# Kernel tuning notes

Hardware: AMD Instinct MI355X
Metric: run time of the kernel (lower is better)

The kernel has to match this reference:

```python
import jax, jax.numpy as jnp
import numpy as np

PIXEL_THRESHOLD = 0.4
FRACTION_THRESHOLD = 0.03
NUM_CLASSES = 20  # cls_idx in [0, 20)
N, H, W = 100, 640, 1280


def setup_inputs() -> dict:
    key = jax.random.key(0)
    k1, k2, k3 = jax.random.split(key, 3)
    cls_prob = jax.random.uniform(k1, (N,), dtype=jnp.float32)
    mask_prob = jax.random.normal(k2, (N, H, W), dtype=jnp.float32)
    cls_idx = jax.random.randint(k3, (N,), 0, NUM_CLASSES, dtype=jnp.int32)
    return {"cls_prob": cls_prob, "mask_prob": mask_prob, "cls_idx": cls_idx}


def reference(cls_prob, mask_prob, cls_idx):
    """Greedy confidence-sorted panoptic mask merging (mask_removal).

    Returns:
      keep:       [N] bool  - whether each (sorted) instance was kept
      kept_masks: [N,H,W]   - assigned raw mask probs (zeros where suppressed/unassigned)
      order:      [N] int   - descending-confidence permutation applied
    """
    # Sort by class confidence, descending (matches np.argsort(...)[::-1])
    order = jnp.argsort(cls_prob)[::-1]
    mp_raw = mask_prob[order]                      # [N,H,W] pre-softmax copy
    mp_soft = jax.nn.softmax(mp_raw, axis=0)       # softmax across instances per pixel
    ci = cls_idx[order]                            # [N]

    h, w = mp_raw.shape[-2:]
    pan0 = jnp.zeros((h, w), dtype=mp_raw.dtype)            # panoptic_image
    mimg0 = jnp.zeros((NUM_CLASSES + 1, h, w), dtype=mp_raw.dtype)  # per-class mask_image

    def step(carry, inp):
        pan, mimg = carry
        prob_s, prob_raw, cidx = inp
        logit = (prob_s >= PIXEL_THRESHOLD).astype(prob_s.dtype)  # binarized mask
        mask_sum = logit.sum()
        curr = mimg[cidx]                                         # [H,W]
        overlap_cnt = ((curr >= 1) & (logit == 1)).sum().astype(prob_s.dtype)
        overlap = overlap_cnt / jnp.maximum(mask_sum, 1.0)
        trivial = logit.max() == logit.min()  # all-zero or all-one mask
        keep = (~trivial) & (mask_sum > 0) & (overlap <= FRACTION_THRESHOLD)
        assign = (pan == 0) & (logit == 1) & keep                 # unclaimed pixels
        kept_mask = jnp.where(assign, prob_raw, 0.0)
        pan = jnp.where(assign, 1.0, pan)
        mimg = mimg.at[cidx].add(jnp.where(assign, logit, 0.0))
        return (pan, mimg), (keep, kept_mask)

    (_, _), (keep, kept_masks) = jax.lax.scan(step, (pan0, mimg0), (mp_soft, mp_raw, ci))
    return keep, kept_masks, order
```

## Files before the change

### kernel.cpp

```cpp
#include <hip/hip_runtime.h>

#define N_INST 100
#define HW_PIX 819200
#define NPAIR (N_INST * N_INST)

struct alignas(16) Ent { int p; int ab; float ra; float rb; };

__global__ __launch_bounds__(128) void k0_sort(
    const float* __restrict__ cls_prob,
    const int* __restrict__ cls_idx,
    int* __restrict__ order,
    int* __restrict__ cls_sorted,
    float* __restrict__ out_order) {
  __shared__ float v[N_INST];
  __shared__ int ordl[N_INST];
  int t = threadIdx.x;
  if (t < N_INST) v[t] = cls_prob[t];
  __syncthreads();
  if (t < N_INST) {
    float mv = v[t];
    int r = 0;
    for (int j = 0; j < N_INST; ++j) {
      float vj = v[j];
      r += (vj > mv) || (vj == mv && j > t);
    }
    ordl[r] = t;
  }
  __syncthreads();
  if (t < N_INST) {
    int o = ordl[t];
    order[t] = o;
    cls_sorted[t] = cls_idx[o];
    out_order[t] = (float)o;
  }
}

__global__ __launch_bounds__(256) void k1_cand(
    const float* __restrict__ mp,
    const int* __restrict__ order,
    unsigned int* __restrict__ masksum,
    unsigned int* __restrict__ paircnt,
    unsigned int* __restrict__ nc,
    Ent* __restrict__ list) {
  int p = blockIdx.x * 256 + threadIdx.x;
  float x[N_INST];
#pragma unroll
  for (int k = 0; k < N_INST; ++k)
    x[k] = mp[(size_t)order[k] * HW_PIX + p];
  float m = x[0];
#pragma unroll
  for (int k = 1; k < N_INST; ++k) m = fmaxf(m, x[k]);
  float denom = 0.0f, e1 = -1.0f, e2 = -1.0f, r1 = 0.0f, r2 = 0.0f;
  int s1 = 0, s2 = 0;
#pragma unroll
  for (int k = 0; k < N_INST; ++k) {
    float e = expf(x[k] - m);
    denom += e;
    if (e > e1)      { e2 = e1; s2 = s1; r2 = r1; e1 = e; s1 = k; r1 = x[k]; }
    else if (e > e2) { e2 = e;  s2 = k;  r2 = x[k]; }
  }
  bool c1 = (e1 / denom) >= 0.4f;
  bool c2 = (e2 / denom) >= 0.4f;
  if (c1) {
    int a = s1, b = 255;
    float ra = r1, rb = 0.0f;
    atomicAdd(&masksum[s1], 1u);
    if (c2) {
      atomicAdd(&masksum[s2], 1u);
      if (s2 < s1) { a = s2; ra = r2; b = s1; rb = r1; }
      else         { b = s2; rb = r2; }
      atomicAdd(&paircnt[a * N_INST + b], 1u);
    }
    unsigned idx = atomicAdd(nc, 1u);
    Ent e; e.p = p; e.ab = a | (b << 8); e.ra = ra; e.rb = rb;
    list[idx] = e;
  }
}

__global__ __launch_bounds__(256) void k2_keep(
    const unsigned int* __restrict__ paircnt,
    const unsigned int* __restrict__ masksum,
    const int* __restrict__ cls_sorted,
    unsigned long long* __restrict__ keepmask,
    float* __restrict__ out_keep) {
  __shared__ unsigned int pl[NPAIR];
  __shared__ unsigned int ms[N_INST];
  __shared__ int cl[N_INST];
  for (int i = threadIdx.x; i < NPAIR; i += 256) pl[i] = paircnt[i];
  if (threadIdx.x < N_INST) {
    ms[threadIdx.x] = masksum[threadIdx.x];
    cl[threadIdx.x] = cls_sorted[threadIdx.x];
  }
  __syncthreads();
  if (threadIdx.x < 64) {
    int l = threadIdx.x;
    int j2 = l + 64;
    int cA = cl[l];
    int cB = (j2 < N_INST) ? cl[j2] : -1;
    bool kA = false, kB = false;
    unsigned long long km0 = 0, km1 = 0;
    for (int s = 0; s < N_INST; ++s) {
      int cs = cl[s];
      unsigned int ov = 0;
      if (l < s && kA && cA == cs) ov += pl[l * N_INST + s];
      if (j2 < s && kB && cB == cs) ov += pl[j2 * N_INST + s];
#pragma unroll
      for (int off = 32; off >= 1; off >>= 1) ov += __shfl_xor((int)ov, off);
      unsigned int m_s = ms[s];
      float overlap = (float)ov / fmaxf((float)m_s, 1.0f);
      bool keep = (m_s > 0u) && (m_s < (unsigned)HW_PIX) && (overlap <= 0.03f);
      if (keep) { if (s < 64) km0 |= 1ull << s; else km1 |= 1ull << (s - 64); }
      if (s == l)  kA = keep;
      if (s == j2) kB = keep;
    }
    if (l == 0) { keepmask[0] = km0; keepmask[1] = km1; }
    out_keep[l] = kA ? 1.0f : 0.0f;
    if (j2 < N_INST) out_keep[j2] = kB ? 1.0f : 0.0f;
  }
}

__global__ __launch_bounds__(256) void k3_scatter(
    const unsigned int* __restrict__ nc,
    const Ent* __restrict__ list,
    const unsigned long long* __restrict__ keepmask,
    float* __restrict__ out_masks) {
  unsigned long long km0 = keepmask[0], km1 = keepmask[1];
  unsigned n = *nc;
  for (unsigned i = blockIdx.x * 256 + threadIdx.x; i < n; i += gridDim.x * 256) {
    Ent e = list[i];
    int a = e.ab & 0xFF;
    int b = (e.ab >> 8) & 0xFF;
    bool ka = (a < 64) ? (((km0 >> a) & 1ull) != 0)
                       : ((a < N_INST) && (((km1 >> (a - 64)) & 1ull) != 0));
    bool kb = (b < 64) ? (((km0 >> b) & 1ull) != 0)
                       : ((b < N_INST) && (((km1 >> (b - 64)) & 1ull) != 0));
    if (ka)      out_masks[(size_t)a * HW_PIX + e.p] = e.ra;
    else if (kb) out_masks[(size_t)b * HW_PIX + e.p] = e.rb;
  }
}

extern "C" void kernel_launch(void* const* d_in, const int* in_sizes, int n_in,
                              void* d_out, int out_size, void* d_ws, size_t ws_size,
                              hipStream_t stream) {
  const float* cls_prob = (const float*)d_in[0];
  const float* mp       = (const float*)d_in[1];
  const int*   cls_idx  = (const int*)d_in[2];
  float* out = (float*)d_out;

  char* ws = (char*)d_ws;
  int* order                   = (int*)(ws + 0);
  int* cls_sorted              = (int*)(ws + 400);
  unsigned long long* keepmask = (unsigned long long*)(ws + 800);
  unsigned int* nc             = (unsigned int*)(ws + 1024);
  unsigned int* masksum        = (unsigned int*)(ws + 2048);
  unsigned int* paircnt        = (unsigned int*)(ws + 4096);
  Ent* list                    = (Ent*)(ws + 65536);

  float* out_keep  = out;
  float* out_masks = out + N_INST;
  float* out_order = out + N_INST + (size_t)N_INST * HW_PIX;

  hipMemsetAsync(ws + 1024, 0, 4096 - 1024 + 40000, stream);
  hipMemsetAsync(out_masks, 0, (size_t)N_INST * HW_PIX * sizeof(float), stream);

  k0_sort<<<1, 128, 0, stream>>>(cls_prob, cls_idx, order, cls_sorted, out_order);
  k1_cand<<<HW_PIX / 256, 256, 0, stream>>>(mp, order, masksum, paircnt, nc, list);
  k2_keep<<<1, 256, 0, stream>>>(paircnt, masksum, cls_sorted, keepmask, out_keep);
  k3_scatter<<<128, 256, 0, stream>>>(nc, list, keepmask, out_masks);
}
```

Before: 610.7 us.

## Replace memset+scatter with dense per-pixel records and a full vectorized output write

The compacted candidate list built with a global atomic counter is replaced by dense per-pixel records holding the winning pair and its raw values. The final kernel now writes the whole output mask tensor with float4 stores, filling zeros itself, so the separate 328MB memset disappears. The candidate kernel also caches the order in shared memory and finds the top-2 on raw logits, so only one exp pass is needed. The cost is extra per-pixel record traffic (about 10MB) in exchange for dropping one full pass over the output.

Result: slower. 889.7 us (+45.7%).

```diff
diff --git a/kernel.cpp b/kernel.cpp
--- a/kernel.cpp
+++ b/kernel.cpp
@@ -3,8 +3,6 @@
 #define N_INST 100
 #define HW_PIX 819200
 #define NPAIR (N_INST * N_INST)
-
-struct alignas(16) Ent { int p; int ab; float ra; float rb; };
 
 __global__ __launch_bounds__(128) void k0_sort(
     const float* __restrict__ cls_prob,
@@ -40,41 +38,46 @@
     const int* __restrict__ order,
     unsigned int* __restrict__ masksum,
     unsigned int* __restrict__ paircnt,
-    unsigned int* __restrict__ nc,
-    Ent* __restrict__ list) {
+    unsigned int* __restrict__ ab_rec,
+    float2* __restrict__ rv_rec) {
+  __shared__ int so[N_INST];
+  if (threadIdx.x < N_INST) so[threadIdx.x] = order[threadIdx.x];
+  __syncthreads();
+
   int p = blockIdx.x * 256 + threadIdx.x;
+
   float x[N_INST];
-#pragma unroll
-  for (int k = 0; k < N_INST; ++k)
-    x[k] = mp[(size_t)order[k] * HW_PIX + p];
-  float m = x[0];
-#pragma unroll
-  for (int k = 1; k < N_INST; ++k) m = fmaxf(m, x[k]);
-  float denom = 0.0f, e1 = -1.0f, e2 = -1.0f, r1 = 0.0f, r2 = 0.0f;
+  float m1 = -3.0e38f, m2 = -3.0e38f;
   int s1 = 0, s2 = 0;
 #pragma unroll
   for (int k = 0; k < N_INST; ++k) {
-    float e = expf(x[k] - m);
-    denom += e;
-    if (e > e1)      { e2 = e1; s2 = s1; r2 = r1; e1 = e; s1 = k; r1 = x[k]; }
-    else if (e > e2) { e2 = e;  s2 = k;  r2 = x[k]; }
+    float xv = mp[(size_t)so[k] * HW_PIX + p];
+    x[k] = xv;
+    if (xv > m1)      { m2 = m1; s2 = s1; m1 = xv; s1 = k; }
+    else if (xv > m2) { m2 = xv; s2 = k; }
   }
-  bool c1 = (e1 / denom) >= 0.4f;
-  bool c2 = (e2 / denom) >= 0.4f;
+  float denom = 0.0f;
+#pragma unroll
+  for (int k = 0; k < N_INST; ++k) denom += expf(x[k] - m1);
+
+  bool c1 = (1.0f / denom) >= 0.4f;
+  bool c2 = (expf(m2 - m1) / denom) >= 0.4f;
+
+  unsigned int abv = 0xFFFFu;
   if (c1) {
     int a = s1, b = 255;
-    float ra = r1, rb = 0.0f;
+    float ra = m1, rb = 0.0f;
     atomicAdd(&masksum[s1], 1u);
     if (c2) {
       atomicAdd(&masksum[s2], 1u);
-      if (s2 < s1) { a = s2; ra = r2; b = s1; rb = r1; }
-      else         { b = s2; rb = r2; }
+      if (s2 < s1) { a = s2; ra = m2; b = s1; rb = m1; }
+      else         { b = s2; rb = m2; }
       atomicAdd(&paircnt[a * N_INST + b], 1u);
     }
-    unsigned idx = atomicAdd(nc, 1u);
-    Ent e; e.p = p; e.ab = a | (b << 8); e.ra = ra; e.rb = rb;
-    list[idx] = e;
+    abv = (unsigned)a | ((unsigned)b << 8);
+    rv_rec[p] = make_float2(ra, rb);
   }
+  ab_rec[p] = abv;
 }
 
 __global__ __launch_bounds__(256) void k2_keep(
@@ -119,23 +122,46 @@
   }
 }
 
-__global__ __launch_bounds__(256) void k3_scatter(
-    const unsigned int* __restrict__ nc,
-    const Ent* __restrict__ list,
+__global__ __launch_bounds__(256) void k3_write(
+    const unsigned int* __restrict__ ab_rec,
+    const float2* __restrict__ rv_rec,
     const unsigned long long* __restrict__ keepmask,
     float* __restrict__ out_masks) {
   unsigned long long km0 = keepmask[0], km1 = keepmask[1];
-  unsigned n = *nc;
-  for (unsigned i = blockIdx.x * 256 + threadIdx.x; i < n; i += gridDim.x * 256) {
-    Ent e = list[i];
-    int a = e.ab & 0xFF;
-    int b = (e.ab >> 8) & 0xFF;
+  int base = (blockIdx.x * 256 + threadIdx.x) * 8;
+  int w[8];
+  float val[8];
+#pragma unroll
+  for (int k = 0; k < 8; ++k) {
+    unsigned int abv = ab_rec[base + k];
+    int a = (int)(abv & 0xFF);
+    int b = (int)((abv >> 8) & 0xFF);
     bool ka = (a < 64) ? (((km0 >> a) & 1ull) != 0)
                        : ((a < N_INST) && (((km1 >> (a - 64)) & 1ull) != 0));
     bool kb = (b < 64) ? (((km0 >> b) & 1ull) != 0)
                        : ((b < N_INST) && (((km1 >> (b - 64)) & 1ull) != 0));
-    if (ka)      out_masks[(size_t)a * HW_PIX + e.p] = e.ra;
-    else if (kb) out_masks[(size_t)b * HW_PIX + e.p] = e.rb;
+    w[k] = ka ? a : (kb ? b : 255);
+    if (w[k] != 255) {
+      float2 rv = rv_rec[base + k];
+      val[k] = ka ? rv.x : rv.y;
+    } else {
+      val[k] = 0.0f;
+    }
+  }
+#pragma unroll 2
+  for (int s = 0; s < N_INST; ++s) {
+    float4 lo, hi;
+    lo.x = (w[0] == s) ? val[0] : 0.0f;
+    lo.y = (w[1] == s) ? val[1] : 0.0f;
+    lo.z = (w[2] == s) ? val[2] : 0.0f;
+    lo.w = (w[3] == s) ? val[3] : 0.0f;
+    hi.x = (w[4] == s) ? val[4] : 0.0f;
+    hi.y = (w[5] == s) ? val[5] : 0.0f;
+    hi.z = (w[6] == s) ? val[6] : 0.0f;
+    hi.w = (w[7] == s) ? val[7] : 0.0f;
+    float* dst = out_masks + (size_t)s * HW_PIX + base;
+    *(float4*)dst = lo;
+    *(float4*)(dst + 4) = hi;
   }
 }
 
@@ -151,20 +177,19 @@
   int* order                   = (int*)(ws + 0);
   int* cls_sorted              = (int*)(ws + 400);
   unsigned long long* keepmask = (unsigned long long*)(ws + 800);
-  unsigned int* nc             = (unsigned int*)(ws + 1024);
-  unsigned int* masksum        = (unsigned int*)(ws + 2048);
-  unsigned int* paircnt        = (unsigned int*)(ws + 4096);
-  Ent* list                    = (Ent*)(ws + 65536);
+  unsigned int* masksum        = (unsigned int*)(ws + 1024);
+  unsigned int* paircnt        = (unsigned int*)(ws + 2048);
+  unsigned int* ab_rec         = (unsigned int*)(ws + 65536);
+  float2* rv_rec               = (float2*)(ws + 65536 + 4 * HW_PIX);
 
   float* out_keep  = out;
   float* out_masks = out + N_INST;
   float* out_order = out + N_INST + (size_t)N_INST * HW_PIX;
 
-  hipMemsetAsync(ws + 1024, 0, 4096 - 1024 + 40000, stream);
-  hipMemsetAsync(out_masks, 0, (size_t)N_INST * HW_PIX * sizeof(float), stream);
+  hipMemsetAsync(ws + 1024, 0, 1024 + 40000, stream);
 
   k0_sort<<<1, 128, 0, stream>>>(cls_prob, cls_idx, order, cls_sorted, out_order);
-  k1_cand<<<HW_PIX / 256, 256, 0, stream>>>(mp, order, masksum, paircnt, nc, list);
+  k1_cand<<<HW_PIX / 256, 256, 0, stream>>>(mp, order, masksum, paircnt, ab_rec, rv_rec);
   k2_keep<<<1, 256, 0, stream>>>(paircnt, masksum, cls_sorted, keepmask, out_keep);
-  k3_scatter<<<128, 256, 0, stream>>>(nc, list, keepmask, out_masks);
+  k3_write<<<HW_PIX / (256 * 8), 256, 0, stream>>>(ab_rec, rv_rec, keepmask, out_masks);
 }
```
